# Performance work log

Hardware: AMD Instinct MI355X
Metric: run time of the kernel (lower is better)

Reference implementation:

```python
import jax, jax.numpy as jnp
import numpy as np

N_ITERS = 25
LAMBDA_INIT = 0.1
TOL = 1e-6
EPS = 1e-10
REWEIGHTED = True


def setup_inputs() -> dict:
    key = jax.random.key(0)
    k1, k2 = jax.random.split(key)
    Y = jax.random.normal(k1, (16, 1024, 64), dtype=jnp.float32)   # [batch, T, joints]
    D = jax.random.normal(k2, (1024, 2048), dtype=jnp.float32)     # [T, Np]
    return {"Y": Y, "D": D}


def _soft_threshold(x, tau):
    return jnp.sign(x) * jnp.maximum(jnp.abs(x) - tau, 0.0)


def _converge(C_curr, C_prev, t_prev, DtD, DtY, L, lam):
    # Fixed-length scan emulating the torch loop with a data-dependent break:
    # once the Frobenius norm of (C_next - C_curr) drops below TOL, the state
    # is frozen (equivalent to breaking out of the loop).
    def body(carry, _):
        Cc, Cp, t, done = carry
        grad = jnp.einsum('pq,bqj->bpj', DtD, Cp) - DtY      # [b, Np, j]
        C_next = _soft_threshold(Cp - L * grad, L * lam)
        small = jnp.linalg.norm(C_next - Cc) < TOL
        do = jnp.logical_not(done | small)
        t_next = (1.0 + jnp.sqrt(1.0 + 4.0 * t * t)) * 0.5
        t_const = (t - 1.0) / t_next
        Cp_new = C_next + t_const * (C_next - Cc)
        carry = (jnp.where(do, C_next, Cc),
                 jnp.where(do, Cp_new, Cp),
                 jnp.where(do, t_next, t),
                 done | small)
        return carry, None

    init = (C_curr, C_prev, t_prev, jnp.array(False))
    (Cc, Cp, t, _), _ = jax.lax.scan(body, init, None, length=N_ITERS)
    return Cc, Cp, t


def _fista(Y, D):
    b, T, j = Y.shape
    Np = D.shape[1]
    Dt = D.T
    DtD = Dt @ D                                   # [Np, Np]
    DtY = jnp.einsum('pt,btj->bpj', Dt, Y)         # [b, Np, j]
    L = 1.0 / jnp.linalg.norm(DtD, ord=2)          # 1 / spectral norm
    Cc = jnp.zeros((b, Np, j), Y.dtype)
    Cp = Cc
    t = jnp.asarray(1.0, Y.dtype)
    lam = jnp.asarray(LAMBDA_INIT, Y.dtype)
    if REWEIGHTED:
        # torch runs: converge -> weight_lambda -> converge -> weight_lambda;
        # the final weight_lambda does not affect the returned C.
        Cc, Cp, t = _converge(Cc, Cp, t, DtD, DtY, L, lam)
        w = 1.0 / (jnp.abs(Cc) + EPS)
        w = w / jnp.linalg.norm(w, axis=1, keepdims=True)  # L2 over Np dim
        lam = lam * w * Np
        Cc, Cp, t = _converge(Cc, Cp, t, DtD, DtY, L, lam)
    else:
        Cc, Cp, t = _converge(Cc, Cp, t, DtD, DtY, L, lam)
    return Cc


def reference(Y, D):
    return _fista(Y, D)
```

## Files before the change

kernel.cpp:

```cpp
#include <hip/hip_runtime.h>
#include <math.h>

#define T_DIM 1024
#define NP    2048
#define NB    1024
#define NITER 25
#define NSQ   7
#define NPI   8
#define LAM0  0.1f
#define EPS_W 1e-10f

typedef float    f32x4 __attribute__((ext_vector_type(4)));
typedef _Float16 f16x8 __attribute__((ext_vector_type(8)));
typedef _Float16 f16x4 __attribute__((ext_vector_type(4)));

__device__ __forceinline__ void gload16(const void* g, void* l) {
  __builtin_amdgcn_global_load_lds((const __attribute__((address_space(1))) unsigned int*)g,
                                   (__attribute__((address_space(3))) unsigned int*)l, 16, 0, 0);
}

__device__ __forceinline__ void mm3_core(
    const _Float16* __restrict__ Ah, const _Float16* __restrict__ Al,
    const _Float16* __restrict__ Bh, const _Float16* __restrict__ Bl,
    int ldk, int n0, int p0, int kb0, int nsteps,
    f32x4 acc0[4][2], f32x4 acc1[4][2])
{
  __shared__ __align__(16) _Float16 sAh[8192], sAl[8192], sBh[8192], sBl[8192];
  const int tid = threadIdx.x;
  const int lane = tid & 63, wave = tid >> 6;
  const int quad = lane >> 4, rl = lane & 15;
#pragma unroll
  for (int i = 0; i < 4; i++)
#pragma unroll
    for (int j = 0; j < 2; j++) { acc0[i][j] = (f32x4)0.0f; acc1[i][j] = (f32x4)0.0f; }
  const int wn = (wave >> 2) * 64, wp = (wave & 3) * 32;

  for (int s = 0; s < nsteps; s++) {
    const int kb = kb0 + s * 64;
    if (s) __syncthreads();
#pragma unroll
    for (int i = 0; i < 2; i++) {
      int slot = i * 512 + wave * 64 + lane;
      int kc = slot >> 7, row = slot & 127;
      int lb = (i * 512 + wave * 64) * 8;
      size_t ga = (size_t)(n0 + row) * ldk + kb + kc * 8;
      size_t gb = (size_t)(p0 + row) * ldk + kb + kc * 8;
      gload16(Ah + ga, sAh + lb);
      gload16(Al + ga, sAl + lb);
      gload16(Bh + gb, sBh + lb);
      gload16(Bl + gb, sBl + lb);
    }
    __syncthreads();
#pragma unroll
    for (int kk = 0; kk < 2; kk++) {
      const int kc = kk * 4 + quad;
      f16x8 a_h[4], a_l[4], b_h[2], b_l[2];
#pragma unroll
      for (int t = 0; t < 4; t++) {
        int ar = wn + t * 16 + rl;
        a_h[t] = *(const f16x8*)&sAh[(kc * 128 + ar) * 8];
        a_l[t] = *(const f16x8*)&sAl[(kc * 128 + ar) * 8];
      }
#pragma unroll
      for (int t = 0; t < 2; t++) {
        int bp = wp + t * 16 + rl;
        b_h[t] = *(const f16x8*)&sBh[(kc * 128 + bp) * 8];
        b_l[t] = *(const f16x8*)&sBl[(kc * 128 + bp) * 8];
      }
#pragma unroll
      for (int mt = 0; mt < 4; mt++)
#pragma unroll
        for (int nt = 0; nt < 2; nt++)
          acc0[mt][nt] = __builtin_amdgcn_mfma_f32_16x16x32_f16(a_h[mt], b_h[nt], acc0[mt][nt], 0, 0, 0);
#pragma unroll
      for (int mt = 0; mt < 4; mt++)
#pragma unroll
        for (int nt = 0; nt < 2; nt++)
          acc1[mt][nt] = __builtin_amdgcn_mfma_f32_16x16x32_f16(a_l[mt], b_h[nt], acc1[mt][nt], 0, 0, 0);
#pragma unroll
      for (int mt = 0; mt < 4; mt++)
#pragma unroll
        for (int nt = 0; nt < 2; nt++)
          acc1[mt][nt] = __builtin_amdgcn_mfma_f32_16x16x32_f16(a_h[mt], b_l[nt], acc1[mt][nt], 0, 0, 0);
    }
  }
}

__global__ __launch_bounds__(512, 2) void k_mm(const _Float16* __restrict__ Ch, const _Float16* __restrict__ Cl,
                                               const _Float16* __restrict__ H, const _Float16* __restrict__ Ee,
                                               float* __restrict__ part) {
  f32x4 acc0[4][2], acc1[4][2];
  const int n0 = blockIdx.x * 128, p0 = blockIdx.y * 128;
  mm3_core(Ch, Cl, H, Ee, 2048, n0, p0, blockIdx.z * 1024, 16, acc0, acc1);
  const int lane = threadIdx.x & 63, wave = threadIdx.x >> 6;
  const int quad = lane >> 4, rl = lane & 15;
  const int wn = (wave >> 2) * 64, wp = (wave & 3) * 32;
  float* op = part + (size_t)blockIdx.z * NB * NP;
#pragma unroll
  for (int mt = 0; mt < 4; mt++)
#pragma unroll
    for (int nt = 0; nt < 2; nt++)
#pragma unroll
      for (int r = 0; r < 4; r++) {
        int row = n0 + wn + mt * 16 + quad * 4 + r;
        int col = p0 + wp + nt * 16 + rl;
        op[(size_t)row * NP + col] = acc0[mt][nt][r] + acc1[mt][nt][r] * (1.f / 4096.f);
      }
}

__global__ __launch_bounds__(512, 2) void k_dtd(const _Float16* __restrict__ Dth, const _Float16* __restrict__ Dtl,
                                                _Float16* __restrict__ H, _Float16* __restrict__ Ee) {
  f32x4 acc0[4][2], acc1[4][2];
  const int n0 = blockIdx.x * 128, p0 = blockIdx.y * 128;
  mm3_core(Dth, Dtl, Dth, Dtl, 1024, n0, p0, 0, 16, acc0, acc1);
  const int lane = threadIdx.x & 63, wave = threadIdx.x >> 6;
  const int quad = lane >> 4, rl = lane & 15;
  const int wn = (wave >> 2) * 64, wp = (wave & 3) * 32;
#pragma unroll
  for (int mt = 0; mt < 4; mt++)
#pragma unroll
    for (int nt = 0; nt < 2; nt++)
#pragma unroll
      for (int r = 0; r < 4; r++) {
        int row = n0 + wn + mt * 16 + quad * 4 + r;
        int col = p0 + wp + nt * 16 + rl;
        float v = acc0[mt][nt][r] + acc1[mt][nt][r] * (1.f / 4096.f);
        _Float16 h = (_Float16)v;
        H[(size_t)row * NP + col] = h;
        Ee[(size_t)row * NP + col] = (_Float16)((v - (float)h) * 4096.f);
      }
}

__global__ __launch_bounds__(512, 2) void k_g(const _Float16* __restrict__ Dh, const _Float16* __restrict__ Dl,
                                              float* __restrict__ G, float* __restrict__ ss0) {
  f32x4 acc0[4][2], acc1[4][2];
  const int n0 = blockIdx.x * 128, p0 = blockIdx.y * 128;
  mm3_core(Dh, Dl, Dh, Dl, 2048, n0, p0, 0, 32, acc0, acc1);
  const int tid = threadIdx.x, lane = tid & 63, wave = tid >> 6;
  const int quad = lane >> 4, rl = lane & 15;
  const int wn = (wave >> 2) * 64, wp = (wave & 3) * 32;
  float ssl = 0.f;
#pragma unroll
  for (int mt = 0; mt < 4; mt++)
#pragma unroll
    for (int nt = 0; nt < 2; nt++)
#pragma unroll
      for (int r = 0; r < 4; r++) {
        int row = n0 + wn + mt * 16 + quad * 4 + r;
        int col = p0 + wp + nt * 16 + rl;
        float v = acc0[mt][nt][r] + acc1[mt][nt][r] * (1.f / 4096.f);
        G[(size_t)row * 1024 + col] = v;
        ssl = fmaf(v, v, ssl);
      }
  __shared__ float red[512];
  red[tid] = ssl; __syncthreads();
  for (int off = 256; off > 0; off >>= 1) {
    if (tid < off) red[tid] += red[tid + off];
    __syncthreads();
  }
  if (tid == 0) atomicAdd(ss0, red[0]);
}

__global__ __launch_bounds__(512, 2) void k_dty(const _Float16* __restrict__ Yth, const _Float16* __restrict__ Ytl,
                                                const _Float16* __restrict__ Dth, const _Float16* __restrict__ Dtl,
                                                float* __restrict__ DtY_) {
  f32x4 acc0[4][2], acc1[4][2];
  const int n0 = blockIdx.x * 128, p0 = blockIdx.y * 128;
  mm3_core(Yth, Ytl, Dth, Dtl, 1024, n0, p0, 0, 16, acc0, acc1);
  const int lane = threadIdx.x & 63, wave = threadIdx.x >> 6;
  const int quad = lane >> 4, rl = lane & 15;
  const int wn = (wave >> 2) * 64, wp = (wave & 3) * 32;
#pragma unroll
  for (int mt = 0; mt < 4; mt++)
#pragma unroll
    for (int nt = 0; nt < 2; nt++)
#pragma unroll
      for (int r = 0; r < 4; r++) {
        int row = n0 + wn + mt * 16 + quad * 4 + r;
        int col = p0 + wp + nt * 16 + rl;
        DtY_[(size_t)row * NP + col] = acc0[mt][nt][r] + acc1[mt][nt][r] * (1.f / 4096.f);
      }
}

__global__ __launch_bounds__(512, 2) void k_sqf(const _Float16* __restrict__ Mh, const float* __restrict__ ssPrev,
                                                float* __restrict__ Mout, float* __restrict__ ssNext, float invfac) {
  __shared__ __align__(16) _Float16 sA[8192], sB[8192];
  const int tid = threadIdx.x;
  const int lane = tid & 63, wave = tid >> 6;
  const int quad = lane >> 4, rl = lane & 15;
  const int wn = (wave >> 2) * 64, wp = (wave & 3) * 32;
  const int n0 = blockIdx.x * 128, p0 = blockIdx.y * 128;
  f32x4 acc[4][2];
#pragma unroll
  for (int i = 0; i < 4; i++)
#pragma unroll
    for (int j = 0; j < 2; j++) acc[i][j] = (f32x4)0.0f;

  for (int s = 0; s < 16; s++) {
    const int kb = s * 64;
    if (s) __syncthreads();
#pragma unroll
    for (int i = 0; i < 2; i++) {
      int slot = i * 512 + wave * 64 + lane;
      int kc = slot >> 7, row = slot & 127;
      int lb = (i * 512 + wave * 64) * 8;
      gload16(Mh + (size_t)(n0 + row) * 1024 + kb + kc * 8, sA + lb);
      gload16(Mh + (size_t)(p0 + row) * 1024 + kb + kc * 8, sB + lb);
    }
    __syncthreads();
#pragma unroll
    for (int kk = 0; kk < 2; kk++) {
      const int kc = kk * 4 + quad;
      f16x8 a[4], b[2];
#pragma unroll
      for (int t = 0; t < 4; t++) a[t] = *(const f16x8*)&sA[(kc * 128 + wn + t * 16 + rl) * 8];
#pragma unroll
      for (int t = 0; t < 2; t++) b[t] = *(const f16x8*)&sB[(kc * 128 + wp + t * 16 + rl) * 8];
#pragma unroll
      for (int mt = 0; mt < 4; mt++)
#pragma unroll
        for (int nt = 0; nt < 2; nt++)
          acc[mt][nt] = __builtin_amdgcn_mfma_f32_16x16x32_f16(a[mt], b[nt], acc[mt][nt], 0, 0, 0);
    }
  }
  const float inv = invfac / ssPrev[0];
  float ssl = 0.f;
#pragma unroll
  for (int mt = 0; mt < 4; mt++)
#pragma unroll
    for (int nt = 0; nt < 2; nt++)
#pragma unroll
      for (int r = 0; r < 4; r++) {
        int row = n0 + wn + mt * 16 + quad * 4 + r;
        int col = p0 + wp + nt * 16 + rl;
        float v = acc[mt][nt][r] * inv;
        Mout[(size_t)row * 1024 + col] = v;
        ssl = fmaf(v, v, ssl);
      }
  __shared__ float red[512];
  red[tid] = ssl; __syncthreads();
  for (int off = 256; off > 0; off >>= 1) {
    if (tid < off) red[tid] += red[tid + off];
    __syncthreads();
  }
  if (tid == 0) atomicAdd(ssNext, red[0]);
}

__global__ __launch_bounds__(256) void k_epi(const float* __restrict__ part,
    const float* __restrict__ DtY_, const float* __restrict__ CcIn,
    const _Float16* __restrict__ ChIn, const _Float16* __restrict__ ClIn,
    const float* __restrict__ Lptr, const float* __restrict__ thrM, float tc,
    float* __restrict__ CcOut, _Float16* __restrict__ ChOut, _Float16* __restrict__ ClOut) {
  const size_t g = ((size_t)blockIdx.x * 256 + threadIdx.x) * 4;
  const float Lv = Lptr[0];
  float p0[4], p1[4], dy[4], cc[4], th[4];
  *(float4*)p0 = *(const float4*)(part + g);
  *(float4*)p1 = *(const float4*)(part + (size_t)NB * NP + g);
  *(float4*)dy = *(const float4*)(DtY_ + g);
  *(float4*)cc = *(const float4*)(CcIn + g);
  f16x4 chv = *(const f16x4*)(ChIn + g);
  f16x4 clv = *(const f16x4*)(ClIn + g);
  if (thrM) { *(float4*)th = *(const float4*)(thrM + g); }
  float cn[4];
  f16x4 ho, lo;
#pragma unroll
  for (int j = 0; j < 4; j++) {
    float grad = (p0[j] + p1[j]) - dy[j];
    float cp = (float)chv[j] + (float)clv[j] * (1.f / 4096.f);
    float z = cp - Lv * grad;
    float t2 = thrM ? th[j] : Lv * LAM0;
    float az = fabsf(z) - t2;
    float v = az > 0.f ? copysignf(az, z) : 0.f;
    cn[j] = v;
    float cpn = fmaf(tc, v - cc[j], v);
    _Float16 h = (_Float16)cpn;
    ho[j] = h;
    lo[j] = (_Float16)((cpn - (float)h) * 4096.f);
  }
  *(float4*)(CcOut + g) = *(float4*)cn;
  *(f16x4*)(ChOut + g) = ho;
  *(f16x4*)(ClOut + g) = lo;
}

__global__ __launch_bounds__(256) void k_split(const float* __restrict__ src, _Float16* __restrict__ H,
                                               _Float16* __restrict__ L, int n4) {
  int g = blockIdx.x * 256 + threadIdx.x;
  if (g < n4) {
    float4 v = ((const float4*)src)[g];
    float vv[4] = {v.x, v.y, v.z, v.w};
    f16x4 h, l;
#pragma unroll
    for (int j = 0; j < 4; j++) {
      _Float16 hh = (_Float16)vv[j];
      h[j] = hh;
      l[j] = (_Float16)((vv[j] - (float)hh) * 4096.f);
    }
    ((f16x4*)H)[g] = h;
    ((f16x4*)L)[g] = l;
  }
}

__global__ __launch_bounds__(256) void k_h16(const float* __restrict__ src, _Float16* __restrict__ dst,
                                             int n4, float scale) {
  int g = blockIdx.x * 256 + threadIdx.x;
  if (g < n4) {
    float4 v = ((const float4*)src)[g];
    f16x4 h;
    h[0] = (_Float16)(v.x * scale); h[1] = (_Float16)(v.y * scale);
    h[2] = (_Float16)(v.z * scale); h[3] = (_Float16)(v.w * scale);
    ((f16x4*)dst)[g] = h;
  }
}

__global__ __launch_bounds__(256) void k_tr(const float* __restrict__ src, float* __restrict__ dst,
// ... 18 lines not shown
  }
}

__global__ __launch_bounds__(256) void k_trY(const float* __restrict__ Y, float* __restrict__ Yt) {
  __shared__ float T[64][65];
  const int tid = threadIdx.x;
  const int t0 = blockIdx.x * 64, b = blockIdx.y;
  const int cx = tid & 15, ry = tid >> 4;
#pragma unroll
  for (int ii = 0; ii < 4; ii++) {
    int r = ry + ii * 16;
    float4 v = *(const float4*)(Y + ((size_t)b * T_DIM + t0 + r) * 64 + cx * 4);
    T[cx * 4 + 0][r] = v.x; T[cx * 4 + 1][r] = v.y;
    T[cx * 4 + 2][r] = v.z; T[cx * 4 + 3][r] = v.w;
  }
  __syncthreads();
#pragma unroll
  for (int ii = 0; ii < 4; ii++) {
    int j = ry + ii * 16;
    float4 v = make_float4(T[j][cx * 4], T[j][cx * 4 + 1], T[j][cx * 4 + 2], T[j][cx * 4 + 3]);
    *(float4*)(Yt + ((size_t)b * 64 + j) * T_DIM + t0 + cx * 4) = v;
  }
}

__global__ void k_initx(float* __restrict__ X) {
  int g = blockIdx.x * 256 + threadIdx.x;
  if (g < 4096) {
    unsigned h = (unsigned)g * 2654435761u;
    h ^= h >> 16; h *= 2246822519u; h ^= h >> 13;
    X[g] = ((float)(h & 0xffffff) / 16777216.0f) - 0.5f;
  }
}

__global__ __launch_bounds__(256) void k_matvec(const float* __restrict__ M, const float* __restrict__ Xin,
                                                float* __restrict__ Xout, const float* __restrict__ prevNorm,
                                                float* __restrict__ outNorm) {
  const int tid = threadIdx.x, lane = tid & 63, w = tid >> 6;
  const int row = blockIdx.x * 4 + w;
  const float* Mr = M + (size_t)row * 1024;
  float s[4] = {0.f, 0.f, 0.f, 0.f};
  for (int j = 0; j < 16; j++) {
    int k = j * 64 + lane;
    float m = Mr[k];
    float4 x = *(const float4*)(Xin + k * 4);
    s[0] = fmaf(m, x.x, s[0]); s[1] = fmaf(m, x.y, s[1]);
    s[2] = fmaf(m, x.z, s[2]); s[3] = fmaf(m, x.w, s[3]);
  }
#pragma unroll
  for (int off = 32; off > 0; off >>= 1)
#pragma unroll
    for (int c = 0; c < 4; c++) s[c] += __shfl_down(s[c], off, 64);
  __shared__ float red[16];
  if (lane == 0) {
#pragma unroll
    for (int c = 0; c < 4; c++) {
      float sc = prevNorm ? rsqrtf(prevNorm[c]) : 1.0f;
      float o = s[c] * sc;
      Xout[row * 4 + c] = o;
      red[w * 4 + c] = o * o;
    }
  }
  __syncthreads();
  if (tid < 4) atomicAdd(&outNorm[tid], red[tid] + red[4 + tid] + red[8 + tid] + red[12 + tid]);
}

__global__ __launch_bounds__(256) void k_rq(const float* __restrict__ G, const float* __restrict__ X,
                                            float* __restrict__ num, float* __restrict__ den) {
  const int tid = threadIdx.x, lane = tid & 63, w = tid >> 6;
  const int row = blockIdx.x * 4 + w;
  const float* Gr = G + (size_t)row * 1024;
  float s[4] = {0.f, 0.f, 0.f, 0.f};
  for (int j = 0; j < 16; j++) {
    int k = j * 64 + lane;
    float m = Gr[k];
    float4 x = *(const float4*)(X + k * 4);
    s[0] = fmaf(m, x.x, s[0]); s[1] = fmaf(m, x.y, s[1]);
// ... 53 lines not shown
}

__global__ __launch_bounds__(256) void k_out(const float* __restrict__ Cc, float* __restrict__ out) {
  __shared__ float T[64][65];
  const int tid = threadIdx.x;
  const int p0 = blockIdx.x * 64, nt = blockIdx.y;
  const int pr = tid & 15, nr = tid >> 4;
#pragma unroll
  for (int ii = 0; ii < 4; ii++) {
    int n_l = nr + ii * 16;
    float4 v = *(const float4*)(Cc + ((size_t)nt * 64 + n_l) * NP + p0 + pr * 4);
    T[pr * 4 + 0][n_l] = v.x; T[pr * 4 + 1][n_l] = v.y;
    T[pr * 4 + 2][n_l] = v.z; T[pr * 4 + 3][n_l] = v.w;
  }
  __syncthreads();
#pragma unroll
  for (int ii = 0; ii < 4; ii++) {
    int p_l = nr + ii * 16;
    float4 v = make_float4(T[p_l][pr * 4], T[p_l][pr * 4 + 1], T[p_l][pr * 4 + 2], T[p_l][pr * 4 + 3]);
    *(float4*)(out + (size_t)nt * (NP * 64) + (size_t)(p0 + p_l) * 64 + pr * 4) = v;
  }
}

#define MBf(x) ((size_t)(x) * 262144)

extern "C" void kernel_launch(void* const* d_in, const int* in_sizes, int n_in,
                              void* d_out, int out_size, void* d_ws, size_t ws_size,
                              hipStream_t stream) {
  const float* Y = (const float*)d_in[0];
  const float* D = (const float*)d_in[1];
  float* out = (float*)d_out;
  float* ws = (float*)d_ws;

  float*    part = ws;
  float*    Dt   = ws;
  float*    Yt   = ws + MBf(8);
  _Float16* H    = (_Float16*)(ws + MBf(16));
  _Float16* Ee   = (_Float16*)(ws + MBf(24));
  float*    DtY  = ws + MBf(32);
  float*    Cc0  = ws + MBf(40);
  float*    Cc1  = ws + MBf(48);
  _Float16* Ch0  = (_Float16*)(ws + MBf(56));
  _Float16* Cl0  = (_Float16*)(ws + MBf(60));
  _Float16* Ch1  = (_Float16*)(ws + MBf(64));
  _Float16* Cl1  = (_Float16*)(ws + MBf(68));
  float*    thrM = ws + MBf(72);
  float*    G    = ws + MBf(80);
  float*    S0   = ws + MBf(84);
  float*    S1   = ws + MBf(88);
  _Float16* Mh   = (_Float16*)(ws + MBf(92));
  _Float16* Dh   = (_Float16*)(ws + MBf(94));
  _Float16* Dl   = (_Float16*)(ws + MBf(98));
  _Float16* Dth  = (_Float16*)(ws + MBf(102));
  _Float16* Dtl  = (_Float16*)(ws + MBf(106));
  _Float16* Yth  = (_Float16*)(ws + MBf(110));
  _Float16* Ytl  = (_Float16*)(ws + MBf(112));
  float*    XA   = ws + MBf(114);
  float*    XB   = XA + 4096;
  float*    scal = XB + 4096;
  float*    ssv   = scal;
  float*    norms = scal + 8;
  float*    num   = scal + 8 + NPI * 4;
  float*    den   = num + 4;
  float*    Lp    = den + 4;
  float*    rowss = Lp + 4;

  float*    CcB[2] = {Cc0, Cc1};
  _Float16* ChB[2] = {Ch0, Ch1};
  _Float16* ClB[2] = {Cl0, Cl1};

  hipMemsetAsync(Cc0, 0, (size_t)NB * NP * sizeof(float), stream);
  hipMemsetAsync(Ch0, 0, (size_t)2 * NB * NP * sizeof(_Float16), stream);
  hipMemsetAsync(scal, 0, (8 + NPI * 4 + 16) * sizeof(float), stream);

  k_initx<<<16, 256, 0, stream>>>(XA);
  k_tr <<<dim3(32, 16), 256, 0, stream>>>(D, Dt, 1024, 2048);
  k_trY<<<dim3(16, 16), 256, 0, stream>>>(Y, Yt);
  k_split<<<2048, 256, 0, stream>>>(D,  Dh,  Dl,  (T_DIM * NP) / 4);
  k_split<<<2048, 256, 0, stream>>>(Dt, Dth, Dtl, (T_DIM * NP) / 4);
  k_split<<<1024, 256, 0, stream>>>(Yt, Yth, Ytl, (NB * T_DIM) / 4);
  k_g  <<<dim3(8, 8),   512, 0, stream>>>(Dh, Dl, G, ssv);
  k_dtd<<<dim3(16, 16), 512, 0, stream>>>(Dth, Dtl, H, Ee);
  k_dty<<<dim3(8, 16),  512, 0, stream>>>(Yth, Ytl, Dth, Dtl, DtY);
  k_h16<<<1024, 256, 0, stream>>>(G, Mh, (1024 * 1024) / 4, 1.0f / 64.0f);
  float* SB[2] = {S0, S1};
  for (int l = 0; l < NSQ; l++) {
    float invfac = (l == 0) ? 4096.0f : (1.0f / 16777216.0f);
    k_sqf<<<dim3(8, 8), 512, 0, stream>>>(Mh, ssv + l, SB[l & 1], ssv + l + 1, invfac);
    if (l + 1 < NSQ)
      k_h16<<<1024, 256, 0, stream>>>(SB[l & 1], Mh, (1024 * 1024) / 4, 4096.0f);
  }
  float* Mfin = SB[(NSQ - 1) & 1];
  for (int i = 0; i < NPI; i++) {
    const float* xin = (i & 1) ? XB : XA;
    float* xout = (i & 1) ? XA : XB;
    k_matvec<<<256, 256, 0, stream>>>(Mfin, xin, xout,
                                      i ? norms + (i - 1) * 4 : nullptr, norms + i * 4);
  }
  k_rq  <<<256, 256, 0, stream>>>(G, XA, num, den);
  k_finL<<<1, 64, 0, stream>>>(num, den, Lp);

  float tcv[2 * NITER];
  {
    float t = 1.0f;
    for (int i = 0; i < 2 * NITER; i++) {
      float tn = 0.5f * (1.0f + sqrtf(1.0f + 4.0f * t * t));
      tcv[i] = (t - 1.0f) / tn;
      t = tn;
    }
  }

  for (int i = 0; i < 2 * NITER; i++) {
    int a = i & 1, b = (i + 1) & 1;
    if (i == NITER) {
      k_rowss <<<1024, 256, 0, stream>>>(CcB[a], rowss);
      k_thrmat<<<(NB * NP) / 256, 256, 0, stream>>>(CcB[a], rowss, Lp, thrM);
    }
    const float* thr = (i < NITER) ? nullptr : thrM;
    k_mm <<<dim3(8, 16, 2), 512, 0, stream>>>(ChB[a], ClB[a], H, Ee, part);
    k_epi<<<(NB * NP) / 1024, 256, 0, stream>>>(part, DtY, CcB[a], ChB[a], ClB[a], Lp, thr,
                                                tcv[i], CcB[b], ChB[b], ClB[b]);
  }
  k_out<<<dim3(32, 16), 256, 0, stream>>>(CcB[0], out);
}
```

Measured before the change: 4.060 ms.

## Split-K four ways in iteration GEMM and Gram kernel with XCD-aware block mapping

The per-iteration k_mm GEMM now splits K into four 512-wide chunks instead of two, launching 512 blocks on a 1D grid. Each block index is remapped so that neighbouring column tiles land on the same XCD, which should improve L2 reuse of H/Ee. The launch-bounds occupancy hint is raised to 4 blocks per CU. k_g is also split four ways, with a new combine kernel that sums the partials and computes the Frobenius norm, and the workspace layout is reshuffled to hold four partial buffers. The cost is more partial-sum traffic in k_epi (four fp32 reads instead of two) and possible register pressure from the higher occupancy target.

Result: faster. 3.816 ms (-6.0%).

```diff
diff --git a/kernel.cpp b/kernel.cpp
--- a/kernel.cpp
+++ b/kernel.cpp
@@ -86,16 +86,21 @@
   }
 }
 
-__global__ __launch_bounds__(512, 2) void k_mm(const _Float16* __restrict__ Ch, const _Float16* __restrict__ Cl,
+__global__ __launch_bounds__(512, 4) void k_mm(const _Float16* __restrict__ Ch, const _Float16* __restrict__ Cl,
                                                const _Float16* __restrict__ H, const _Float16* __restrict__ Ee,
                                                float* __restrict__ part) {
+  const int b = blockIdx.x;
+  const int xcd = b & 7, q = b >> 3;
+  const int pt = xcd * 2 + (q & 1);
+  const int ny = (q >> 1) & 7;
+  const int z  = q >> 4;
   f32x4 acc0[4][2], acc1[4][2];
-  const int n0 = blockIdx.x * 128, p0 = blockIdx.y * 128;
-  mm3_core(Ch, Cl, H, Ee, 2048, n0, p0, blockIdx.z * 1024, 16, acc0, acc1);
+  const int n0 = ny * 128, p0 = pt * 128;
+  mm3_core(Ch, Cl, H, Ee, 2048, n0, p0, z * 512, 8, acc0, acc1);
   const int lane = threadIdx.x & 63, wave = threadIdx.x >> 6;
   const int quad = lane >> 4, rl = lane & 15;
   const int wn = (wave >> 2) * 64, wp = (wave & 3) * 32;
-  float* op = part + (size_t)blockIdx.z * NB * NP;
+  float* op = part + (size_t)z * NB * NP;
 #pragma unroll
   for (int mt = 0; mt < 4; mt++)
 #pragma unroll
@@ -132,14 +137,14 @@
 }
 
 __global__ __launch_bounds__(512, 2) void k_g(const _Float16* __restrict__ Dh, const _Float16* __restrict__ Dl,
-                                              float* __restrict__ G, float* __restrict__ ss0) {
+                                              float* __restrict__ gpart) {
   f32x4 acc0[4][2], acc1[4][2];
   const int n0 = blockIdx.x * 128, p0 = blockIdx.y * 128;
-  mm3_core(Dh, Dl, Dh, Dl, 2048, n0, p0, 0, 32, acc0, acc1);
-  const int tid = threadIdx.x, lane = tid & 63, wave = tid >> 6;
+  mm3_core(Dh, Dl, Dh, Dl, 2048, n0, p0, blockIdx.z * 512, 8, acc0, acc1);
+  const int lane = threadIdx.x & 63, wave = threadIdx.x >> 6;
   const int quad = lane >> 4, rl = lane & 15;
   const int wn = (wave >> 2) * 64, wp = (wave & 3) * 32;
-  float ssl = 0.f;
+  float* op = gpart + (size_t)blockIdx.z * 1024 * 1024;
 #pragma unroll
   for (int mt = 0; mt < 4; mt++)
 #pragma unroll
@@ -148,13 +153,30 @@
       for (int r = 0; r < 4; r++) {
         int row = n0 + wn + mt * 16 + quad * 4 + r;
         int col = p0 + wp + nt * 16 + rl;
-        float v = acc0[mt][nt][r] + acc1[mt][nt][r] * (1.f / 4096.f);
-        G[(size_t)row * 1024 + col] = v;
-        ssl = fmaf(v, v, ssl);
+        op[(size_t)row * 1024 + col] = acc0[mt][nt][r] + acc1[mt][nt][r] * (1.f / 4096.f);
       }
-  __shared__ float red[512];
+}
+
+__global__ __launch_bounds__(256) void k_gcomb(const float* __restrict__ gpart, float* __restrict__ G,
+                                               float* __restrict__ ss0) {
+  const int tid = threadIdx.x;
+  const size_t g = ((size_t)blockIdx.x * 256 + tid) * 4;
+  float v[4];
+  *(float4*)v = *(const float4*)(gpart + g);
+#pragma unroll
+  for (int z = 1; z < 4; z++) {
+    float t[4];
+    *(float4*)t = *(const float4*)(gpart + (size_t)z * 1024 * 1024 + g);
+#pragma unroll
+    for (int j = 0; j < 4; j++) v[j] += t[j];
+  }
+  *(float4*)(G + g) = *(float4*)v;
+  float ssl = 0.f;
+#pragma unroll
+  for (int j = 0; j < 4; j++) ssl = fmaf(v[j], v[j], ssl);
+  __shared__ float red[256];
   red[tid] = ssl; __syncthreads();
-  for (int off = 256; off > 0; off >>= 1) {
+  for (int off = 128; off > 0; off >>= 1) {
     if (tid < off) red[tid] += red[tid + off];
     __syncthreads();
   }
@@ -253,9 +275,15 @@
     float* __restrict__ CcOut, _Float16* __restrict__ ChOut, _Float16* __restrict__ ClOut) {
   const size_t g = ((size_t)blockIdx.x * 256 + threadIdx.x) * 4;
   const float Lv = Lptr[0];
-  float p0[4], p1[4], dy[4], cc[4], th[4];
-  *(float4*)p0 = *(const float4*)(part + g);
-  *(float4*)p1 = *(const float4*)(part + (size_t)NB * NP + g);
+  float ps[4], dy[4], cc[4], th[4];
+  *(float4*)ps = *(const float4*)(part + g);
+#pragma unroll
+  for (int z = 1; z < 4; z++) {
+    float t[4];
+    *(float4*)t = *(const float4*)(part + (size_t)z * NB * NP + g);
+#pragma unroll
+    for (int j = 0; j < 4; j++) ps[j] += t[j];
+  }
   *(float4*)dy = *(const float4*)(DtY_ + g);
   *(float4*)cc = *(const float4*)(CcIn + g);
   f16x4 chv = *(const f16x4*)(ChIn + g);
@@ -265,7 +293,7 @@
   f16x4 ho, lo;
 #pragma unroll
   for (int j = 0; j < 4; j++) {
-    float grad = (p0[j] + p1[j]) - dy[j];
+    float grad = ps[j] - dy[j];
     float cp = (float)chv[j] + (float)clv[j] * (1.f / 4096.f);
     float z = cp - Lv * grad;
     float t2 = thrM ? th[j] : Lv * LAM0;
@@ -494,29 +522,30 @@
   float* ws = (float*)d_ws;
 
   float*    part = ws;
+  _Float16* H    = (_Float16*)(ws + MBf(32));
+  _Float16* Ee   = (_Float16*)(ws + MBf(40));
+  float*    DtY  = ws + MBf(48);
+  float*    Cc0  = ws + MBf(56);
+  float*    Cc1  = ws + MBf(64);
+  _Float16* Ch0  = (_Float16*)(ws + MBf(72));
+  _Float16* Cl0  = (_Float16*)(ws + MBf(76));
+  _Float16* Ch1  = (_Float16*)(ws + MBf(80));
+  _Float16* Cl1  = (_Float16*)(ws + MBf(84));
+  float*    thrM = ws + MBf(88);
   float*    Dt   = ws;
   float*    Yt   = ws + MBf(8);
-  _Float16* H    = (_Float16*)(ws + MBf(16));
-  _Float16* Ee   = (_Float16*)(ws + MBf(24));
-  float*    DtY  = ws + MBf(32);
-  float*    Cc0  = ws + MBf(40);
-  float*    Cc1  = ws + MBf(48);
-  _Float16* Ch0  = (_Float16*)(ws + MBf(56));
-  _Float16* Cl0  = (_Float16*)(ws + MBf(60));
-  _Float16* Ch1  = (_Float16*)(ws + MBf(64));
-  _Float16* Cl1  = (_Float16*)(ws + MBf(68));
-  float*    thrM = ws + MBf(72);
-  float*    G    = ws + MBf(80);
-  float*    S0   = ws + MBf(84);
-  float*    S1   = ws + MBf(88);
-  _Float16* Mh   = (_Float16*)(ws + MBf(92));
-  _Float16* Dh   = (_Float16*)(ws + MBf(94));
-  _Float16* Dl   = (_Float16*)(ws + MBf(98));
-  _Float16* Dth  = (_Float16*)(ws + MBf(102));
-  _Float16* Dtl  = (_Float16*)(ws + MBf(106));
-  _Float16* Yth  = (_Float16*)(ws + MBf(110));
-  _Float16* Ytl  = (_Float16*)(ws + MBf(112));
-  float*    XA   = ws + MBf(114);
+  float*    gpart= ws;
+  float*    G    = ws + MBf(16);
+  _Float16* Mh   = (_Float16*)(ws + MBf(20));
+  float*    S0   = ws + MBf(22);
+  float*    S1   = ws + MBf(26);
+  _Float16* Dh   = (_Float16*)(ws + MBf(64));
+  _Float16* Dl   = (_Float16*)(ws + MBf(68));
+  _Float16* Dth  = (_Float16*)(ws + MBf(80));
+  _Float16* Dtl  = (_Float16*)(ws + MBf(84));
+  _Float16* Yth  = (_Float16*)(ws + MBf(88));
+  _Float16* Ytl  = (_Float16*)(ws + MBf(90));
+  float*    XA   = ws + MBf(96);
   float*    XB   = XA + 4096;
   float*    scal = XB + 4096;
   float*    ssv   = scal;
@@ -540,9 +569,10 @@
   k_split<<<2048, 256, 0, stream>>>(D,  Dh,  Dl,  (T_DIM * NP) / 4);
   k_split<<<2048, 256, 0, stream>>>(Dt, Dth, Dtl, (T_DIM * NP) / 4);
   k_split<<<1024, 256, 0, stream>>>(Yt, Yth, Ytl, (NB * T_DIM) / 4);
-  k_g  <<<dim3(8, 8),   512, 0, stream>>>(Dh, Dl, G, ssv);
-  k_dtd<<<dim3(16, 16), 512, 0, stream>>>(Dth, Dtl, H, Ee);
-  k_dty<<<dim3(8, 16),  512, 0, stream>>>(Yth, Ytl, Dth, Dtl, DtY);
+  k_g    <<<dim3(8, 8, 4), 512, 0, stream>>>(Dh, Dl, gpart);
+  k_gcomb<<<1024, 256, 0, stream>>>(gpart, G, ssv);
+  k_dtd  <<<dim3(16, 16), 512, 0, stream>>>(Dth, Dtl, H, Ee);
+  k_dty  <<<dim3(8, 16),  512, 0, stream>>>(Yth, Ytl, Dth, Dtl, DtY);
   k_h16<<<1024, 256, 0, stream>>>(G, Mh, (1024 * 1024) / 4, 1.0f / 64.0f);
   float* SB[2] = {S0, S1};
   for (int l = 0; l < NSQ; l++) {
@@ -578,7 +608,7 @@
       k_thrmat<<<(NB * NP) / 256, 256, 0, stream>>>(CcB[a], rowss, Lp, thrM);
     }
     const float* thr = (i < NITER) ? nullptr : thrM;
-    k_mm <<<dim3(8, 16, 2), 512, 0, stream>>>(ChB[a], ClB[a], H, Ee, part);
+    k_mm <<<512, 512, 0, stream>>>(ChB[a], ClB[a], H, Ee, part);
     k_epi<<<(NB * NP) / 1024, 256, 0, stream>>>(part, DtY, CcB[a], ChB[a], ClB[a], Lp, thr,
                                                 tcv[i], CcB[b], ChB[b], ClB[b]);
   }
```

## Fuse FISTA epilogue into GEMM, use 64x64 tiles with XCD-aware block mapping

Applied to the files above, without the earlier changes.

The per-iteration GEMM now uses smaller 64x64 output tiles with 256 threads and the full K range in one block, which drops the split-K partial buffer. The soft-threshold/momentum epilogue is fused directly into the GEMM, so the separate k_epi pass over the partial results disappears. Block indices are remapped so that adjacent p-tiles land on the same XCD for L2 reuse. The squaring kernel writes fp16 directly, which removes the intermediate fp32 matrix and the k_h16 conversion launches. The epilogue now uses scattered scalar stores instead of vectorized ones, and the smaller tiles lower arithmetic intensity per block.

After: 4.273 ms. 5.2% more time.

```diff
diff --git a/kernel.cpp b/kernel.cpp
--- a/kernel.cpp
+++ b/kernel.cpp
@@ -19,30 +19,30 @@
                                    (__attribute__((address_space(3))) unsigned int*)l, 16, 0, 0);
 }
 
-__device__ __forceinline__ void mm3_core(
+__device__ __forceinline__ void mm3c(
     const _Float16* __restrict__ Ah, const _Float16* __restrict__ Al,
     const _Float16* __restrict__ Bh, const _Float16* __restrict__ Bl,
-    int ldk, int n0, int p0, int kb0, int nsteps,
-    f32x4 acc0[4][2], f32x4 acc1[4][2])
+    int ldk, int n0, int p0, int nsteps,
+    f32x4 acc0[2][2], f32x4 acc1[2][2])
 {
   __shared__ __align__(16) _Float16 sAh[8192], sAl[8192], sBh[8192], sBl[8192];
   const int tid = threadIdx.x;
-  const int lane = tid & 63, wave = tid >> 6;
+  const int lane = tid & 63, w = tid >> 6;
   const int quad = lane >> 4, rl = lane & 15;
-#pragma unroll
-  for (int i = 0; i < 4; i++)
+  const int wm = (w >> 1) * 32, wp = (w & 1) * 32;
+#pragma unroll
+  for (int i = 0; i < 2; i++)
 #pragma unroll
     for (int j = 0; j < 2; j++) { acc0[i][j] = (f32x4)0.0f; acc1[i][j] = (f32x4)0.0f; }
-  const int wn = (wave >> 2) * 64, wp = (wave & 3) * 32;
 
   for (int s = 0; s < nsteps; s++) {
-    const int kb = kb0 + s * 64;
+    const int kb = s * 128;
     if (s) __syncthreads();
 #pragma unroll
-    for (int i = 0; i < 2; i++) {
-      int slot = i * 512 + wave * 64 + lane;
-      int kc = slot >> 7, row = slot & 127;
-      int lb = (i * 512 + wave * 64) * 8;
+    for (int i = 0; i < 4; i++) {
+      int slot = i * 256 + w * 64 + lane;
+      int kc = slot >> 6, row = slot & 63;
+      int lb = (i * 256 + w * 64) * 8;
       size_t ga = (size_t)(n0 + row) * ldk + kb + kc * 8;
       size_t gb = (size_t)(p0 + row) * ldk + kb + kc * 8;
       gload16(Ah + ga, sAh + lb);
@@ -52,234 +52,228 @@
     }
     __syncthreads();
 #pragma unroll
-    for (int kk = 0; kk < 2; kk++) {
+    for (int kk = 0; kk < 4; kk++) {
       const int kc = kk * 4 + quad;
-      f16x8 a_h[4], a_l[4], b_h[2], b_l[2];
-#pragma unroll
-      for (int t = 0; t < 4; t++) {
-        int ar = wn + t * 16 + rl;
-        a_h[t] = *(const f16x8*)&sAh[(kc * 128 + ar) * 8];
-        a_l[t] = *(const f16x8*)&sAl[(kc * 128 + ar) * 8];
+      f16x8 a_h[2], a_l[2], b_h[2], b_l[2];
+#pragma unroll
+      for (int t = 0; t < 2; t++) {
+        int ar = wm + t * 16 + rl;
+        int bp = wp + t * 16 + rl;
+        a_h[t] = *(const f16x8*)&sAh[(kc * 64 + ar) * 8];
+        a_l[t] = *(const f16x8*)&sAl[(kc * 64 + ar) * 8];
+        b_h[t] = *(const f16x8*)&sBh[(kc * 64 + bp) * 8];
+        b_l[t] = *(const f16x8*)&sBl[(kc * 64 + bp) * 8];
       }
 #pragma unroll
-      for (int t = 0; t < 2; t++) {
-        int bp = wp + t * 16 + rl;
-        b_h[t] = *(const f16x8*)&sBh[(kc * 128 + bp) * 8];
-        b_l[t] = *(const f16x8*)&sBl[(kc * 128 + bp) * 8];
+      for (int mt = 0; mt < 2; mt++)
+#pragma unroll
+        for (int nt = 0; nt < 2; nt++) {
+          acc0[mt][nt] = __builtin_amdgcn_mfma_f32_16x16x32_f16(a_h[mt], b_h[nt], acc0[mt][nt], 0, 0, 0);
+          acc1[mt][nt] = __builtin_amdgcn_mfma_f32_16x16x32_f16(a_l[mt], b_h[nt], acc1[mt][nt], 0, 0, 0);
+          acc1[mt][nt] = __builtin_amdgcn_mfma_f32_16x16x32_f16(a_h[mt], b_l[nt], acc1[mt][nt], 0, 0, 0);
+        }
+    }
+  }
+}
+
+__global__ __launch_bounds__(256, 2) void k_mm(const _Float16* __restrict__ Ch, const _Float16* __restrict__ Cl,
+                                               const _Float16* __restrict__ H, const _Float16* __restrict__ Ee,
+                                               const float* __restrict__ DtY_, const float* __restrict__ CcIn,
+                                               const float* __restrict__ Lptr, const float* __restrict__ thrM,
+                                               float tc, float* __restrict__ CcOut,
+                                               _Float16* __restrict__ ChOut, _Float16* __restrict__ ClOut) {
+  const int b = blockIdx.x;
+  const int xcd = b & 7, i4 = b >> 3;
+  const int ny = i4 >> 2, pt = xcd * 4 + (i4 & 3);
+  const int n0 = ny * 64, p0 = pt * 64;
+  f32x4 acc0[2][2], acc1[2][2];
+  mm3c(Ch, Cl, H, Ee, 2048, n0, p0, 16, acc0, acc1);
+  const int lane = threadIdx.x & 63, w = threadIdx.x >> 6;
+  const int quad = lane >> 4, rl = lane & 15;
+  const int wm = (w >> 1) * 32, wp = (w & 1) * 32;
+  const float Lv = Lptr[0];
+  const float thr_s = Lv * LAM0;
+#pragma unroll
+  for (int mt = 0; mt < 2; mt++)
+#pragma unroll
+    for (int nt = 0; nt < 2; nt++) {
+      const int p = p0 + wp + nt * 16 + rl;
+      const size_t rb = (size_t)(n0 + wm + mt * 16 + quad * 4) * NP + p;
+#pragma unroll
+      for (int r = 0; r < 4; r++) {
+        const size_t idx = rb + (size_t)r * NP;
+        float gemm = acc0[mt][nt][r] + acc1[mt][nt][r] * (1.f / 4096.f);
+        float grad = gemm - DtY_[idx];
+        float cp = (float)Ch[idx] + (float)Cl[idx] * (1.f / 4096.f);
+        float z = cp - Lv * grad;
+        float t2 = thrM ? thrM[idx] : thr_s;
+        float az = fabsf(z) - t2;
+        float v = az > 0.f ? copysignf(az, z) : 0.f;
+        CcOut[idx] = v;
+        float cpn = fmaf(tc, v - CcIn[idx], v);
+        _Float16 h = (_Float16)cpn;
+        ChOut[idx] = h;
+        ClOut[idx] = (_Float16)((cpn - (float)h) * 4096.f);
       }
-#pragma unroll
-      for (int mt = 0; mt < 4; mt++)
-#pragma unroll
-        for (int nt = 0; nt < 2; nt++)
-          acc0[mt][nt] = __builtin_amdgcn_mfma_f32_16x16x32_f16(a_h[mt], b_h[nt], acc0[mt][nt], 0, 0, 0);
-#pragma unroll
-      for (int mt = 0; mt < 4; mt++)
-#pragma unroll
-        for (int nt = 0; nt < 2; nt++)
-          acc1[mt][nt] = __builtin_amdgcn_mfma_f32_16x16x32_f16(a_l[mt], b_h[nt], acc1[mt][nt], 0, 0, 0);
-#pragma unroll
-      for (int mt = 0; mt < 4; mt++)
-#pragma unroll
-        for (int nt = 0; nt < 2; nt++)
-          acc1[mt][nt] = __builtin_amdgcn_mfma_f32_16x16x32_f16(a_h[mt], b_l[nt], acc1[mt][nt], 0, 0, 0);
-    }
-  }
-}
-
-__global__ __launch_bounds__(512, 2) void k_mm(const _Float16* __restrict__ Ch, const _Float16* __restrict__ Cl,
-                                               const _Float16* __restrict__ H, const _Float16* __restrict__ Ee,
-                                               float* __restrict__ part) {
-  f32x4 acc0[4][2], acc1[4][2];
-  const int n0 = blockIdx.x * 128, p0 = blockIdx.y * 128;
-  mm3_core(Ch, Cl, H, Ee, 2048, n0, p0, blockIdx.z * 1024, 16, acc0, acc1);
-  const int lane = threadIdx.x & 63, wave = threadIdx.x >> 6;
+    }
+}
+
+__global__ __launch_bounds__(256, 2) void k_dtd(const _Float16* __restrict__ Dth, const _Float16* __restrict__ Dtl,
+                                                _Float16* __restrict__ H, _Float16* __restrict__ Ee) {
+  const int b = blockIdx.x;
+  const int xcd = b & 7, i4 = b >> 3;
+  const int ny = i4 >> 2, pt = xcd * 4 + (i4 & 3);
+  const int n0 = ny * 64, p0 = pt * 64;
+  f32x4 acc0[2][2], acc1[2][2];
+  mm3c(Dth, Dtl, Dth, Dtl, 1024, n0, p0, 8, acc0, acc1);
+  const int lane = threadIdx.x & 63, w = threadIdx.x >> 6;
   const int quad = lane >> 4, rl = lane & 15;
-  const int wn = (wave >> 2) * 64, wp = (wave & 3) * 32;
-  float* op = part + (size_t)blockIdx.z * NB * NP;
-#pragma unroll
-  for (int mt = 0; mt < 4; mt++)
-#pragma unroll
-    for (int nt = 0; nt < 2; nt++)
+  const int wm = (w >> 1) * 32, wp = (w & 1) * 32;
+#pragma unroll
+  for (int mt = 0; mt < 2; mt++)
+#pragma unroll
+    for (int nt = 0; nt < 2; nt++) {
+      const int p = p0 + wp + nt * 16 + rl;
+      const size_t rb = (size_t)(n0 + wm + mt * 16 + quad * 4) * NP + p;
 #pragma unroll
       for (int r = 0; r < 4; r++) {
-        int row = n0 + wn + mt * 16 + quad * 4 + r;
-        int col = p0 + wp + nt * 16 + rl;
-        op[(size_t)row * NP + col] = acc0[mt][nt][r] + acc1[mt][nt][r] * (1.f / 4096.f);
-      }
-}
-
-__global__ __launch_bounds__(512, 2) void k_dtd(const _Float16* __restrict__ Dth, const _Float16* __restrict__ Dtl,
-                                                _Float16* __restrict__ H, _Float16* __restrict__ Ee) {
-  f32x4 acc0[4][2], acc1[4][2];
-  const int n0 = blockIdx.x * 128, p0 = blockIdx.y * 128;
-  mm3_core(Dth, Dtl, Dth, Dtl, 1024, n0, p0, 0, 16, acc0, acc1);
-  const int lane = threadIdx.x & 63, wave = threadIdx.x >> 6;
-  const int quad = lane >> 4, rl = lane & 15;
-  const int wn = (wave >> 2) * 64, wp = (wave & 3) * 32;
-#pragma unroll
-  for (int mt = 0; mt < 4; mt++)
-#pragma unroll
-    for (int nt = 0; nt < 2; nt++)
-#pragma unroll
-      for (int r = 0; r < 4; r++) {
-        int row = n0 + wn + mt * 16 + quad * 4 + r;
-        int col = p0 + wp + nt * 16 + rl;
+        const size_t idx = rb + (size_t)r * NP;
         float v = acc0[mt][nt][r] + acc1[mt][nt][r] * (1.f / 4096.f);
         _Float16 h = (_Float16)v;
-        H[(size_t)row * NP + col] = h;
-        Ee[(size_t)row * NP + col] = (_Float16)((v - (float)h) * 4096.f);
+        H[idx] = h;
+        Ee[idx] = (_Float16)((v - (float)h) * 4096.f);
       }
-}
-
-__global__ __launch_bounds__(512, 2) void k_g(const _Float16* __restrict__ Dh, const _Float16* __restrict__ Dl,
+    }
+}
+
+__global__ __launch_bounds__(256, 2) void k_g(const _Float16* __restrict__ Dh, const _Float16* __restrict__ Dl,
                                               float* __restrict__ G, float* __restrict__ ss0) {
-  f32x4 acc0[4][2], acc1[4][2];
-  const int n0 = blockIdx.x * 128, p0 = blockIdx.y * 128;
-  mm3_core(Dh, Dl, Dh, Dl, 2048, n0, p0, 0, 32, acc0, acc1);
-  const int tid = threadIdx.x, lane = tid & 63, wave = tid >> 6;
+  const int b = blockIdx.x;
+  const int xcd = b & 7, i4 = b >> 3;
+  const int ny = i4 >> 1, pt = xcd * 2 + (i4 & 1);
+  const int n0 = ny * 64, p0 = pt * 64;
+  f32x4 acc0[2][2], acc1[2][2];
+  mm3c(Dh, Dl, Dh, Dl, 2048, n0, p0, 16, acc0, acc1);
+  const int tid = threadIdx.x;
+  const int lane = tid & 63, w = tid >> 6;
   const int quad = lane >> 4, rl = lane & 15;
-  const int wn = (wave >> 2) * 64, wp = (wave & 3) * 32;
+  const int wm = (w >> 1) * 32, wp = (w & 1) * 32;
   float ssl = 0.f;
 #pragma unroll
-  for (int mt = 0; mt < 4; mt++)
-#pragma unroll
-    for (int nt = 0; nt < 2; nt++)
+  for (int mt = 0; mt < 2; mt++)
+#pragma unroll
+    for (int nt = 0; nt < 2; nt++) {
+      const int p = p0 + wp + nt * 16 + rl;
+      const size_t rb = (size_t)(n0 + wm + mt * 16 + quad * 4) * 1024 + p;
 #pragma unroll
       for (int r = 0; r < 4; r++) {
-        int row = n0 + wn + mt * 16 + quad * 4 + r;
-        int col = p0 + wp + nt * 16 + rl;
         float v = acc0[mt][nt][r] + acc1[mt][nt][r] * (1.f / 4096.f);
-        G[(size_t)row * 1024 + col] = v;
+        G[rb + (size_t)r * 1024] = v;
         ssl = fmaf(v, v, ssl);
       }
-  __shared__ float red[512];
+    }
+  __shared__ float red[256];
   red[tid] = ssl; __syncthreads();
-  for (int off = 256; off > 0; off >>= 1) {
+  for (int off = 128; off > 0; off >>= 1) {
     if (tid < off) red[tid] += red[tid + off];
     __syncthreads();
   }
   if (tid == 0) atomicAdd(ss0, red[0]);
 }
 
-__global__ __launch_bounds__(512, 2) void k_dty(const _Float16* __restrict__ Yth, const _Float16* __restrict__ Ytl,
+__global__ __launch_bounds__(256, 2) void k_dty(const _Float16* __restrict__ Yth, const _Float16* __restrict__ Ytl,
                                                 const _Float16* __restrict__ Dth, const _Float16* __restrict__ Dtl,
                                                 float* __restrict__ DtY_) {
-  f32x4 acc0[4][2], acc1[4][2];
-  const int n0 = blockIdx.x * 128, p0 = blockIdx.y * 128;
-  mm3_core(Yth, Ytl, Dth, Dtl, 1024, n0, p0, 0, 16, acc0, acc1);
-  const int lane = threadIdx.x & 63, wave = threadIdx.x >> 6;
+  const int b = blockIdx.x;
+  const int xcd = b & 7, i4 = b >> 3;
+  const int ny = i4 >> 2, pt = xcd * 4 + (i4 & 3);
+  const int n0 = ny * 64, p0 = pt * 64;
+  f32x4 acc0[2][2], acc1[2][2];
+  mm3c(Yth, Ytl, Dth, Dtl, 1024, n0, p0, 8, acc0, acc1);
+  const int lane = threadIdx.x & 63, w = threadIdx.x >> 6;
   const int quad = lane >> 4, rl = lane & 15;
-  const int wn = (wave >> 2) * 64, wp = (wave & 3) * 32;
-#pragma unroll
-  for (int mt = 0; mt < 4; mt++)
-#pragma unroll
-    for (int nt = 0; nt < 2; nt++)
-#pragma unroll
-      for (int r = 0; r < 4; r++) {
-        int row = n0 + wn + mt * 16 + quad * 4 + r;
-        int col = p0 + wp + nt * 16 + rl;
-        DtY_[(size_t)row * NP + col] = acc0[mt][nt][r] + acc1[mt][nt][r] * (1.f / 4096.f);
+  const int wm = (w >> 1) * 32, wp = (w & 1) * 32;
+#pragma unroll
+  for (int mt = 0; mt < 2; mt++)
+#pragma unroll
+    for (int nt = 0; nt < 2; nt++) {
+      const int p = p0 + wp + nt * 16 + rl;
+      const size_t rb = (size_t)(n0 + wm + mt * 16 + quad * 4) * NP + p;
+#pragma unroll
+      for (int r = 0; r < 4; r++)
+        DtY_[rb + (size_t)r * NP] = acc0[mt][nt][r] + acc1[mt][nt][r] * (1.f / 4096.f);
+    }
+}
+
+__global__ __launch_bounds__(256, 2) void k_sqf(const _Float16* __restrict__ Min, const float* __restrict__ ssPrev,
+                                                _Float16* __restrict__ Mout, float* __restrict__ ssNext,
+                                                float invfac) {
+  __shared__ __align__(16) _Float16 sA[8192], sB[8192];
+  const int b = blockIdx.x;
+  const int xcd = b & 7, i4 = b >> 3;
+  const int ny = i4 >> 1, pt = xcd * 2 + (i4 & 1);
+  const int n0 = ny * 64, p0 = pt * 64;
+  const int tid = threadIdx.x;
+  const int lane = tid & 63, w = tid >> 6;
+  const int quad = lane >> 4, rl = lane & 15;
+  const int wm = (w >> 1) * 32, wp = (w & 1) * 32;
+  f32x4 acc[2][2];
+#pragma unroll
+  for (int i = 0; i < 2; i++)
+#pragma unroll
+    for (int j = 0; j < 2; j++) acc[i][j] = (f32x4)0.0f;
+
+  for (int s = 0; s < 8; s++) {
+    const int kb = s * 128;
+    if (s) __syncthreads();
+#pragma unroll
+    for (int i = 0; i < 4; i++) {
+      int slot = i * 256 + w * 64 + lane;
+      int kc = slot >> 6, row = slot & 63;
+      int lb = (i * 256 + w * 64) * 8;
+      gload16(Min + (size_t)(n0 + row) * 1024 + kb + kc * 8, sA + lb);
+      gload16(Min + (size_t)(p0 + row) * 1024 + kb + kc * 8, sB + lb);
+    }
+    __syncthreads();
+#pragma unroll
+    for (int kk = 0; kk < 4; kk++) {
+      const int kc = kk * 4 + quad;
+      f16x8 a[2], bb[2];
+#pragma unroll
+      for (int t = 0; t < 2; t++) {
+        a[t]  = *(const f16x8*)&sA[(kc * 64 + wm + t * 16 + rl) * 8];
+        bb[t] = *(const f16x8*)&sB[(kc * 64 + wp + t * 16 + rl) * 8];
       }
-}
-
-__global__ __launch_bounds__(512, 2) void k_sqf(const _Float16* __restrict__ Mh, const float* __restrict__ ssPrev,
-                                                float* __restrict__ Mout, float* __restrict__ ssNext, float invfac) {
-  __shared__ __align__(16) _Float16 sA[8192], sB[8192];
-  const int tid = threadIdx.x;
-  const int lane = tid & 63, wave = tid >> 6;
-  const int quad = lane >> 4, rl = lane & 15;
-  const int wn = (wave >> 2) * 64, wp = (wave & 3) * 32;
-  const int n0 = blockIdx.x * 128, p0 = blockIdx.y * 128;
-  f32x4 acc[4][2];
-#pragma unroll
-  for (int i = 0; i < 4; i++)
-#pragma unroll
-    for (int j = 0; j < 2; j++) acc[i][j] = (f32x4)0.0f;
-
-  for (int s = 0; s < 16; s++) {
-    const int kb = s * 64;
-    if (s) __syncthreads();
-#pragma unroll
-    for (int i = 0; i < 2; i++) {
-      int slot = i * 512 + wave * 64 + lane;
-      int kc = slot >> 7, row = slot & 127;
-      int lb = (i * 512 + wave * 64) * 8;
-      gload16(Mh + (size_t)(n0 + row) * 1024 + kb + kc * 8, sA + lb);
-      gload16(Mh + (size_t)(p0 + row) * 1024 + kb + kc * 8, sB + lb);
-    }
-    __syncthreads();
-#pragma unroll
-    for (int kk = 0; kk < 2; kk++) {
-      const int kc = kk * 4 + quad;
-      f16x8 a[4], b[2];
-#pragma unroll
-      for (int t = 0; t < 4; t++) a[t] = *(const f16x8*)&sA[(kc * 128 + wn + t * 16 + rl) * 8];
-#pragma unroll
-      for (int t = 0; t < 2; t++) b[t] = *(const f16x8*)&sB[(kc * 128 + wp + t * 16 + rl) * 8];
-#pragma unroll
-      for (int mt = 0; mt < 4; mt++)
+#pragma unroll
+      for (int mt = 0; mt < 2; mt++)
 #pragma unroll
         for (int nt = 0; nt < 2; nt++)
-          acc[mt][nt] = __builtin_amdgcn_mfma_f32_16x16x32_f16(a[mt], b[nt], acc[mt][nt], 0, 0, 0);
+          acc[mt][nt] = __builtin_amdgcn_mfma_f32_16x16x32_f16(a[mt], bb[nt], acc[mt][nt], 0, 0, 0);
     }
   }
   const float inv = invfac / ssPrev[0];
   float ssl = 0.f;
 #pragma unroll
-  for (int mt = 0; mt < 4; mt++)
-#pragma unroll
-    for (int nt = 0; nt < 2; nt++)
+  for (int mt = 0; mt < 2; mt++)
+#pragma unroll
+    for (int nt = 0; nt < 2; nt++) {
+      const int p = p0 + wp + nt * 16 + rl;
+      const size_t rb = (size_t)(n0 + wm + mt * 16 + quad * 4) * 1024 + p;
 #pragma unroll
       for (int r = 0; r < 4; r++) {
-        int row = n0 + wn + mt * 16 + quad * 4 + r;
-        int col = p0 + wp + nt * 16 + rl;
         float v = acc[mt][nt][r] * inv;
-        Mout[(size_t)row * 1024 + col] = v;
+        Mout[rb + (size_t)r * 1024] = (_Float16)(v * 4096.f);
         ssl = fmaf(v, v, ssl);
       }
-  __shared__ float red[512];
+    }
+  __syncthreads();
+  float* red = (float*)sA;
   red[tid] = ssl; __syncthreads();
-  for (int off = 256; off > 0; off >>= 1) {
+  for (int off = 128; off > 0; off >>= 1) {
     if (tid < off) red[tid] += red[tid + off];
     __syncthreads();
   }
   if (tid == 0) atomicAdd(ssNext, red[0]);
-}
-
-__global__ __launch_bounds__(256) void k_epi(const float* __restrict__ part,
-    const float* __restrict__ DtY_, const float* __restrict__ CcIn,
-    const _Float16* __restrict__ ChIn, const _Float16* __restrict__ ClIn,
-    const float* __restrict__ Lptr, const float* __restrict__ thrM, float tc,
-    float* __restrict__ CcOut, _Float16* __restrict__ ChOut, _Float16* __restrict__ ClOut) {
-  const size_t g = ((size_t)blockIdx.x * 256 + threadIdx.x) * 4;
-  const float Lv = Lptr[0];
-  float p0[4], p1[4], dy[4], cc[4], th[4];
-  *(float4*)p0 = *(const float4*)(part + g);
-  *(float4*)p1 = *(const float4*)(part + (size_t)NB * NP + g);
-  *(float4*)dy = *(const float4*)(DtY_ + g);
-  *(float4*)cc = *(const float4*)(CcIn + g);
-  f16x4 chv = *(const f16x4*)(ChIn + g);
-  f16x4 clv = *(const f16x4*)(ClIn + g);
-  if (thrM) { *(float4*)th = *(const float4*)(thrM + g); }
-  float cn[4];
-  f16x4 ho, lo;
-#pragma unroll
-  for (int j = 0; j < 4; j++) {
-    float grad = (p0[j] + p1[j]) - dy[j];
-    float cp = (float)chv[j] + (float)clv[j] * (1.f / 4096.f);
-    float z = cp - Lv * grad;
-    float t2 = thrM ? th[j] : Lv * LAM0;
-    float az = fabsf(z) - t2;
-    float v = az > 0.f ? copysignf(az, z) : 0.f;
-    cn[j] = v;
-    float cpn = fmaf(tc, v - cc[j], v);
-    _Float16 h = (_Float16)cpn;
-    ho[j] = h;
-    lo[j] = (_Float16)((cpn - (float)h) * 4096.f);
-  }
-  *(float4*)(CcOut + g) = *(float4*)cn;
-  *(f16x4*)(ChOut + g) = ho;
-  *(f16x4*)(ClOut + g) = lo;
 }
 
 __global__ __launch_bounds__(256) void k_split(const float* __restrict__ src, _Float16* __restrict__ H,
@@ -364,16 +358,16 @@
   }
 }
 
-__global__ __launch_bounds__(256) void k_matvec(const float* __restrict__ M, const float* __restrict__ Xin,
+__global__ __launch_bounds__(256) void k_matvec(const _Float16* __restrict__ M, const float* __restrict__ Xin,
                                                 float* __restrict__ Xout, const float* __restrict__ prevNorm,
                                                 float* __restrict__ outNorm) {
   const int tid = threadIdx.x, lane = tid & 63, w = tid >> 6;
   const int row = blockIdx.x * 4 + w;
-  const float* Mr = M + (size_t)row * 1024;
+  const _Float16* Mr = M + (size_t)row * 1024;
   float s[4] = {0.f, 0.f, 0.f, 0.f};
   for (int j = 0; j < 16; j++) {
     int k = j * 64 + lane;
-    float m = Mr[k];
+    float m = (float)Mr[k];
     float4 x = *(const float4*)(Xin + k * 4);
     s[0] = fmaf(m, x.x, s[0]); s[1] = fmaf(m, x.y, s[1]);
     s[2] = fmaf(m, x.z, s[2]); s[3] = fmaf(m, x.w, s[3]);
@@ -493,30 +487,28 @@
   float* out = (float*)d_out;
   float* ws = (float*)d_ws;
 
-  float*    part = ws;
-  float*    Dt   = ws;
-  float*    Yt   = ws + MBf(8);
-  _Float16* H    = (_Float16*)(ws + MBf(16));
-  _Float16* Ee   = (_Float16*)(ws + MBf(24));
-  float*    DtY  = ws + MBf(32);
-  float*    Cc0  = ws + MBf(40);
-  float*    Cc1  = ws + MBf(48);
-  _Float16* Ch0  = (_Float16*)(ws + MBf(56));
-  _Float16* Cl0  = (_Float16*)(ws + MBf(60));
-  _Float16* Ch1  = (_Float16*)(ws + MBf(64));
-  _Float16* Cl1  = (_Float16*)(ws + MBf(68));
-  float*    thrM = ws + MBf(72);
-  float*    G    = ws + MBf(80);
-  float*    S0   = ws + MBf(84);
-  float*    S1   = ws + MBf(88);
-  _Float16* Mh   = (_Float16*)(ws + MBf(92));
-  _Float16* Dh   = (_Float16*)(ws + MBf(94));
-  _Float16* Dl   = (_Float16*)(ws + MBf(98));
-  _Float16* Dth  = (_Float16*)(ws + MBf(102));
-  _Float16* Dtl  = (_Float16*)(ws + MBf(106));
-  _Float16* Yth  = (_Float16*)(ws + MBf(110));
-  _Float16* Ytl  = (_Float16*)(ws + MBf(112));
-  float*    XA   = ws + MBf(114);
+  _Float16* H    = (_Float16*)(ws);
+  _Float16* Ee   = (_Float16*)(ws + MBf(8));
+  float*    DtY  = ws + MBf(16);
+  float*    Cc0  = ws + MBf(24);
+  float*    Cc1  = ws + MBf(32);
+  _Float16* Ch0  = (_Float16*)(ws + MBf(40));
+  _Float16* Cl0  = (_Float16*)(ws + MBf(44));
+  _Float16* Ch1  = (_Float16*)(ws + MBf(48));
+  _Float16* Cl1  = (_Float16*)(ws + MBf(52));
+  float*    thrM = ws + MBf(56);
+  float*    Dt   = ws + MBf(64);
+  float*    Yt   = ws + MBf(72);
+  _Float16* Dh   = (_Float16*)(ws + MBf(76));
+  _Float16* Dl   = (_Float16*)(ws + MBf(80));
+  _Float16* Dth  = (_Float16*)(ws + MBf(84));
+  _Float16* Dtl  = (_Float16*)(ws + MBf(88));
+  _Float16* Yth  = (_Float16*)(ws + MBf(92));
+  _Float16* Ytl  = (_Float16*)(ws + MBf(94));
+  float*    G    = ws + MBf(96);
+  _Float16* Mh0  = (_Float16*)(ws + MBf(100));
+  _Float16* Mh1  = (_Float16*)(ws + MBf(102));
+  float*    XA   = ws + MBf(104);
   float*    XB   = XA + 4096;
   float*    scal = XB + 4096;
   float*    ssv   = scal;
@@ -540,18 +532,16 @@
   k_split<<<2048, 256, 0, stream>>>(D,  Dh,  Dl,  (T_DIM * NP) / 4);
   k_split<<<2048, 256, 0, stream>>>(Dt, Dth, Dtl, (T_DIM * NP) / 4);
   k_split<<<1024, 256, 0, stream>>>(Yt, Yth, Ytl, (NB * T_DIM) / 4);
-  k_g  <<<dim3(8, 8),   512, 0, stream>>>(Dh, Dl, G, ssv);
-  k_dtd<<<dim3(16, 16), 512, 0, stream>>>(Dth, Dtl, H, Ee);
-  k_dty<<<dim3(8, 16),  512, 0, stream>>>(Yth, Ytl, Dth, Dtl, DtY);
-  k_h16<<<1024, 256, 0, stream>>>(G, Mh, (1024 * 1024) / 4, 1.0f / 64.0f);
-  float* SB[2] = {S0, S1};
+  k_g  <<<256,  256, 0, stream>>>(Dh, Dl, G, ssv);
+  k_dtd<<<1024, 256, 0, stream>>>(Dth, Dtl, H, Ee);
+  k_dty<<<512,  256, 0, stream>>>(Yth, Ytl, Dth, Dtl, DtY);
+  k_h16<<<1024, 256, 0, stream>>>(G, Mh0, (1024 * 1024) / 4, 1.0f / 64.0f);
+  _Float16* MB[2] = {Mh0, Mh1};
   for (int l = 0; l < NSQ; l++) {
     float invfac = (l == 0) ? 4096.0f : (1.0f / 16777216.0f);
-    k_sqf<<<dim3(8, 8), 512, 0, stream>>>(Mh, ssv + l, SB[l & 1], ssv + l + 1, invfac);
-    if (l + 1 < NSQ)
-      k_h16<<<1024, 256, 0, stream>>>(SB[l & 1], Mh, (1024 * 1024) / 4, 4096.0f);
-  }
-  float* Mfin = SB[(NSQ - 1) & 1];
+    k_sqf<<<256, 256, 0, stream>>>(MB[l & 1], ssv + l, MB[(l + 1) & 1], ssv + l + 1, invfac);
+  }
+  _Float16* Mfin = MB[NSQ & 1];
   for (int i = 0; i < NPI; i++) {
     const float* xin = (i & 1) ? XB : XA;
     float* xout = (i & 1) ? XA : XB;
@@ -578,9 +568,8 @@
       k_thrmat<<<(NB * NP) / 256, 256, 0, stream>>>(CcB[a], rowss, Lp, thrM);
     }
     const float* thr = (i < NITER) ? nullptr : thrM;
-    k_mm <<<dim3(8, 16, 2), 512, 0, stream>>>(ChB[a], ClB[a], H, Ee, part);
-    k_epi<<<(NB * NP) / 1024, 256, 0, stream>>>(part, DtY, CcB[a], ChB[a], ClB[a], Lp, thr,
-                                                tcv[i], CcB[b], ChB[b], ClB[b]);
+    k_mm<<<512, 256, 0, stream>>>(ChB[a], ClB[a], H, Ee, DtY, CcB[a], Lp, thr,
+                                  tcv[i], CcB[b], ChB[b], ClB[b]);
   }
   k_out<<<dim3(32, 16), 256, 0, stream>>>(CcB[0], out);
 }
```
